# Optimization experiments

Measured on AMD Instinct MI355X. Metric: run time of the kernel, lower is better.

The kernel has to match this reference:

```python
import jax, jax.numpy as jnp
import numpy as np

D_MODEL, N_HEADS, E_LAYERS, D_FF, FACTOR, REP = 128, 8, 5, 64, 3, 128


def setup_inputs() -> dict:
    key = jax.random.key(0)
    ks = jax.random.split(key, 8)
    B, L = 8, 4096
    s = 0.02
    E = E_LAYERS
    def p(k, shape):
        return jax.random.normal(k, shape, jnp.float32) * s
    return dict(
        x=jax.random.normal(ks[0], (B, D_MODEL, L), jnp.float32),
        Wq=p(ks[1], (E, D_MODEL, D_MODEL)), bq=jnp.zeros((E, D_MODEL), jnp.float32),
        Wk=p(ks[2], (E, D_MODEL, D_MODEL)), bk=jnp.zeros((E, D_MODEL), jnp.float32),
        Wv=p(ks[3], (E, D_MODEL, D_MODEL)), bv=jnp.zeros((E, D_MODEL), jnp.float32),
        Wo=p(ks[4], (E, D_MODEL, D_MODEL)), bo=jnp.zeros((E, D_MODEL), jnp.float32),
        W1=p(ks[5], (E, D_FF, D_MODEL)), b1=jnp.zeros((E, D_FF), jnp.float32),
        W2=p(ks[6], (E, D_MODEL, D_FF)), b2=jnp.zeros((E, D_MODEL), jnp.float32),
        ln1_w=jnp.ones((E, D_MODEL), jnp.float32), ln1_b=jnp.zeros((E, D_MODEL), jnp.float32),
        ln2_w=jnp.ones((E, D_MODEL), jnp.float32), ln2_b=jnp.zeros((E, D_MODEL), jnp.float32),
        lnf_w=jnp.ones((D_MODEL,), jnp.float32), lnf_b=jnp.zeros((D_MODEL,), jnp.float32),
        Wp=p(ks[7], (D_MODEL, REP)), bp=jnp.zeros((REP,), jnp.float32),
    )


def _ln(x, w, b, eps=1e-5):
    m = jnp.mean(x, axis=-1, keepdims=True)
    v = jnp.mean((x - m) ** 2, axis=-1, keepdims=True)
    return (x - m) * jax.lax.rsqrt(v + eps) * w + b


def _prob_attn(Q, K, V, key):
    """ProbSparse self-attention (mask_flag=False). Q,K,V: [B,H,L,Eh]."""
    B, H, L, Eh = Q.shape
    c = min(int(FACTOR * np.ceil(np.log(L))), L)  # U_part == u for self-attn
    # sample c keys per query position (shared across batch/head, like torch.randint)
    idx = jax.random.randint(key, (L, c), 0, L)
    Ks = K[:, :, idx, :]                                   # [B,H,L,c,Eh]
    QKs = jnp.einsum('bhle,bhlue->bhlu', Q, Ks)            # sampled scores
    M = QKs.max(-1) - QKs.sum(-1) / L                      # sparsity measure [B,H,L]
    _, top = jax.lax.top_k(M, c)                           # top-u query indices [B,H,c]
    Qr = jnp.take_along_axis(Q, top[..., None], axis=2)    # [B,H,c,Eh]
    scores = jnp.einsum('bhue,bhke->bhuk', Qr, K) * (1.0 / np.sqrt(Eh))
    attn = jax.nn.softmax(scores, axis=-1)                 # [B,H,c,L]
    upd = jnp.einsum('bhuk,bhke->bhue', attn, V)           # [B,H,c,Eh]
    # lazy context: mean of V for non-selected queries
    ctx = jnp.broadcast_to(V.mean(axis=2, keepdims=True), Q.shape)
    bi = jnp.arange(B)[:, None, None]
    hi = jnp.arange(H)[None, :, None]
    ctx = ctx.at[bi, hi, top].set(upd)
    return ctx


def reference(x, Wq, bq, Wk, bk, Wv, bv, Wo, bo, W1, b1, W2, b2,
              ln1_w, ln1_b, ln2_w, ln2_b, lnf_w, lnf_b, Wp, bp):
    B, _, L = x.shape
    Eh = D_MODEL // N_HEADS
    h = jnp.transpose(x, (0, 2, 1))                        # [B,L,D]
    base = jax.random.key(42)
    for l in range(E_LAYERS):
        q = (h @ Wq[l].T + bq[l]).reshape(B, L, N_HEADS, Eh).transpose(0, 2, 1, 3)
        k = (h @ Wk[l].T + bk[l]).reshape(B, L, N_HEADS, Eh).transpose(0, 2, 1, 3)
        v = (h @ Wv[l].T + bv[l]).reshape(B, L, N_HEADS, Eh).transpose(0, 2, 1, 3)
        ctx = _prob_attn(q, k, v, jax.random.fold_in(base, l))
        ctx = ctx.transpose(0, 2, 1, 3).reshape(B, L, D_MODEL)
        h = h + (ctx @ Wo[l].T + bo[l])                    # residual (dropout off)
        h = _ln(h, ln1_w[l], ln1_b[l])
        # 1x1 conv FFN == per-token linear
        y = jax.nn.gelu(h @ W1[l].T + b1[l], approximate=False)
        y = y @ W2[l].T + b2[l]
        h = _ln(h + y, ln2_w[l], ln2_b[l])
    h = _ln(h, lnf_w, lnf_b)
    out = h @ Wp + bp                                      # [B,L,REP]
    return jnp.transpose(out, (0, 2, 1))                   # [B,REP,L]
```

## Files before the change

kernel.cpp:

```cpp
#include <hip/hip_runtime.h>
#include <stdint.h>
#include <math.h>

#define DM   128
#define NH   8
#define EHD  16
#define NLAY 5
#define DFF  64
#define NREP 128
#define NB   8
#define SL   4096
#define NC   27
#define NBH  (NB*NH)
#define NROWS (NB*SL)

typedef _Float16 f16;
typedef f16 f16x8 __attribute__((ext_vector_type(8)));
typedef float f32x16 __attribute__((ext_vector_type(16)));

__device__ __forceinline__ uint32_t rotl32(uint32_t v, int d) {
  return (v << d) | (v >> (32 - d));
}

__device__ __forceinline__ void tf2x32(uint32_t k0, uint32_t k1,
                                       uint32_t x0, uint32_t x1,
                                       uint32_t &o0, uint32_t &o1) {
  uint32_t ks2 = k0 ^ k1 ^ 0x1BD11BDAu;
  x0 += k0; x1 += k1;
#define TFR(r) { x0 += x1; x1 = rotl32(x1, (r)); x1 ^= x0; }
  TFR(13) TFR(15) TFR(26) TFR(6)
  x0 += k1; x1 += ks2 + 1u;
  TFR(17) TFR(29) TFR(16) TFR(24)
  x0 += ks2; x1 += k0 + 2u;
  TFR(13) TFR(15) TFR(26) TFR(6)
  x0 += k0; x1 += k1 + 3u;
  TFR(17) TFR(29) TFR(16) TFR(24)
  x0 += k1; x1 += ks2 + 4u;
  TFR(13) TFR(15) TFR(26) TFR(6)
  x0 += ks2; x1 += k0 + 5u;
#undef TFR
  o0 = x0; o1 = x1;
}

__global__ void gen_bits_kernel(uint32_t* __restrict__ bits, int layer) {
  int i = blockIdx.x * blockDim.x + threadIdx.x;
  if (i >= SL * NC) return;
  uint32_t ka, kb, k2a, k2b, y0, y1;
  tf2x32(0u, 42u, 0u, (uint32_t)layer, ka, kb);
  tf2x32(ka, kb, 0u, 1u, k2a, k2b);
  tf2x32(k2a, k2b, 0u, (uint32_t)i, y0, y1);
  bits[i] = y0 ^ y1;
}

__global__ __launch_bounds__(256) void transpose_x_kernel(const float* __restrict__ x,
                                                          float* __restrict__ h) {
  __shared__ float t[32][33];
  int tid = threadIdx.x;
  int tx = tid & 31, ty = tid >> 5;
  int l0 = blockIdx.x * 32, d0 = blockIdx.y * 32, b = blockIdx.z;
#pragma unroll
  for (int j = 0; j < 4; ++j) {
    int d = d0 + ty + 8 * j;
    t[ty + 8 * j][tx] = x[((size_t)b * DM + d) * SL + l0 + tx];
  }
  __syncthreads();
#pragma unroll
  for (int j = 0; j < 4; ++j) {
    int l = l0 + ty + 8 * j;
    h[((size_t)b * SL + l) * DM + d0 + tx] = t[tx][ty + 8 * j];
  }
}

#define PACK_TOTAL 425984
__global__ __launch_bounds__(256) void prep_weights(
    const float* __restrict__ Wq, const float* __restrict__ Wk,
    const float* __restrict__ Wv, const float* __restrict__ Wo,
    const float* __restrict__ W1, const float* __restrict__ W2,
    const float* __restrict__ Wp, f16* __restrict__ phi, f16* __restrict__ plo) {
  int idx = blockIdx.x * 256 + threadIdx.x;
  if (idx >= PACK_TOTAL) return;
  const float* src; int K, KS16, lsh; int f; bool transp = false;
  if (idx >= 409600) { f = idx - 409600; src = Wp; K = 128; KS16 = 8; lsh = 3; transp = true; }
  else {
    int layer = idx / 81920; int r = idx - layer * 81920;
    if      (r < 16384) { src = Wq + layer * 16384; f = r;         K = 128; KS16 = 8; lsh = 3; }
    else if (r < 32768) { src = Wk + layer * 16384; f = r - 16384; K = 128; KS16 = 8; lsh = 3; }
    else if (r < 49152) { src = Wv + layer * 16384; f = r - 32768; K = 128; KS16 = 8; lsh = 3; }
    else if (r < 65536) { src = Wo + layer * 16384; f = r - 49152; K = 128; KS16 = 8; lsh = 3; }
    else if (r < 73728) { src = W1 + layer * 8192;  f = r - 65536; K = 128; KS16 = 8; lsh = 3; }
    else                { src = W2 + layer * 8192;  f = r - 73728; K = 64;  KS16 = 4; lsh = 2; }
  }
  int j = f & 7, lane = (f >> 3) & 63, rest = f >> 9;
  int ks = rest & (KS16 - 1), nt = rest >> lsh;
  int n = nt * 32 + (lane & 31);
  int kk = ks * 16 + ((lane >> 5) & 1) * 8 + j;
  float x = transp ? src[(size_t)kk * 128 + n] : src[(size_t)n * K + kk];
  f16 h = (f16)x;
  phi[idx] = h;
  plo[idx] = (f16)(x - (float)h);
}

template<int NT32, int KS16, int SRC, int EPI>
__global__ __launch_bounds__(256, 2) void gemm_fused(
    const float* __restrict__ Asrc, const f16* __restrict__ phi,
    const f16* __restrict__ plo,
    const float* __restrict__ bias0, const float* __restrict__ bias1,
    const float* __restrict__ bias2,
    float* out0, float* out1, float* out2,
    const float* __restrict__ gw, const float* __restrict__ gb,
    const float* hres) {
  constexpr int NGW = NT32 / 2;
  constexpr int K = KS16 * 16;
  __shared__ f16x8 Alds[2 * 2 * KS16 * 64];
  __shared__ f16x8 Blds[NT32 * KS16 * 64];
  __shared__ float red[64 * 4];
  int tid = threadIdx.x, lane = tid & 63, wid = tid >> 6;
  int mg = wid >> 1, ng = wid & 1;
  int row0 = blockIdx.x * 64;

  if constexpr (SRC == 0 || SRC == 1) {
    constexpr int OCT = 64 * (K / 8);
    for (int o = tid; o < OCT; o += 256) {
      int row = o / (K / 8);
      int k0 = (o % (K / 8)) * 8;
      float4 f0, f1;
      if constexpr (SRC == 0) {
        const float* s = Asrc + (size_t)(row0 + row) * K + k0;
        f0 = *(const float4*)(s);
        f1 = *(const float4*)(s + 4);
      } else {
        int gr = row0 + row; int bb = gr >> 12, ll = gr & (SL - 1);
        int head = k0 >> 4, e0 = k0 & 15;
        const float* s = Asrc + (((size_t)(bb * NH + head) * SL + ll) * EHD + e0);
        f0 = *(const float4*)(s);
        f1 = *(const float4*)(s + 4);
      }
      f16x8 vh, vl;
      float xs[8] = {f0.x, f0.y, f0.z, f0.w, f1.x, f1.y, f1.z, f1.w};
#pragma unroll
      for (int j = 0; j < 8; ++j) {
        f16 hh = (f16)xs[j];
        vh[j] = hh;
        vl[j] = (f16)(xs[j] - (float)hh);
      }
      int al = (row & 31) | (((k0 >> 3) & 1) << 5);
      int ks = k0 >> 4, mt = row >> 5;
      Alds[((0 * 2 + mt) * KS16 + ks) * 64 + al] = vh;
      Alds[((1 * 2 + mt) * KS16 + ks) * 64 + al] = vl;
    }
  } else {
    int row = tid >> 2, q4 = tid & 3;
    const float* s = Asrc + (size_t)(row0 + row) * 128 + q4 * 32;
    float r[32];
#pragma unroll
    for (int i = 0; i < 8; ++i) {
      float4 f = *(const float4*)(s + 4 * i);
      r[4 * i] = f.x; r[4 * i + 1] = f.y; r[4 * i + 2] = f.z; r[4 * i + 3] = f.w;
    }
    float sm = 0.f, s2 = 0.f;
#pragma unroll
    for (int i = 0; i < 32; ++i) { sm += r[i]; s2 += r[i] * r[i]; }
    sm += __shfl_xor(sm, 1, 4); sm += __shfl_xor(sm, 2, 4);
    s2 += __shfl_xor(s2, 1, 4); s2 += __shfl_xor(s2, 2, 4);
    float mean = sm * (1.f / 128.f);
    float var = s2 * (1.f / 128.f) - mean * mean;
    float rstd = 1.0f / sqrtf(var + 1e-5f);
#pragma unroll
    for (int i = 0; i < 32; ++i) {
      int kk = q4 * 32 + i;
      r[i] = (r[i] - mean) * rstd * gw[kk] + gb[kk];
    }
#pragma unroll
    for (int i = 0; i < 4; ++i) {
      int k0 = q4 * 32 + i * 8;
      f16x8 vh, vl;
#pragma unroll
      for (int j = 0; j < 8; ++j) {
        float x = r[8 * i + j];
        f16 hh = (f16)x;
        vh[j] = hh;
        vl[j] = (f16)(x - (float)hh);
      }
      int al = (row & 31) | (((k0 >> 3) & 1) << 5);
      int ks = k0 >> 4, mt = row >> 5;
      Alds[((0 * 2 + mt) * KS16 + ks) * 64 + al] = vh;
      Alds[((1 * 2 + mt) * KS16 + ks) * 64 + al] = vl;
    }
  }

  constexpr int NMAT = (EPI == 0) ? 3 : 1;
  constexpr int BCNT = NT32 * KS16 * 64;

#define STAGE_B(SRCPTR)                                        \
  {                                                            \
    const float4* bsrc = (const float4*)(SRCPTR);              \
    float4* bdst = (float4*)Blds;                              \
    _Pragma("unroll")                                          \
    for (int i = 0; i < BCNT / 256; ++i) bdst[tid + i * 256] = bsrc[tid + i * 256]; \
  }

#define GEMM_PASS(ASEL)                                                         \
  _Pragma("unroll")                                                             \
  for (int ks = 0; ks < KS16; ++ks) {                                           \
    f16x8 afr = Alds[(((ASEL) * 2 + mg) * KS16 + ks) * 64 + lane];              \
    _Pragma("unroll")                                                           \
    for (int g = 0; g < NGW; ++g) {                                             \
      f16x8 bfr = Blds[((ng * NGW + g) * KS16 + ks) * 64 + lane];               \
      acc[g] = __builtin_amdgcn_mfma_f32_32x32x16_f16(afr, bfr, acc[g], 0, 0, 0); \
    }                                                                           \
  }

  for (int m = 0; m < NMAT; ++m) {
    if (m) __syncthreads();
    STAGE_B(phi + m * 16384)
    __syncthreads();
    f32x16 acc[NGW];
#pragma unroll
    for (int g = 0; g < NGW; ++g)
#pragma unroll
      for (int j = 0; j < 16; ++j) acc[g][j] = 0.f;
    GEMM_PASS(0)
    GEMM_PASS(1)
    __syncthreads();
    STAGE_B(plo + m * 16384)
    __syncthreads();
    GEMM_PASS(0)

    int hi4 = 4 * (lane >> 5);
    if constexpr (EPI == 0) {
      const float* bm = (m == 0) ? bias0 : (m == 1) ? bias1 : bias2;
      float* om = (m == 0) ? out0 : (m == 1) ? out1 : out2;
#pragma unroll
      for (int g = 0; g < NGW; ++g) {
        int col = ng * (NGW * 32) + g * 32 + (lane & 31);
        float bv = bm[col];
        int head = col >> 4, e = col & 15;
#pragma unroll
        for (int reg = 0; reg < 16; ++reg) {
          int row_l = (reg & 3) + 8 * (reg >> 2) + hi4;
          int grow = row0 + mg * 32 + row_l;
          int bb = grow >> 12, ll = grow & (SL - 1);
          om[((size_t)(bb * NH + head) * SL + ll) * EHD + e] = acc[g][reg] + bv;
        }
      }
    } else if constexpr (EPI == 3) {
#pragma unroll
      for (int g = 0; g < NGW; ++g) {
        int col = ng * (NGW * 32) + g * 32 + (lane & 31);
        float bv = bias0[col];
#pragma unroll
        for (int reg = 0; reg < 16; ++reg) {
          int row_l = (reg & 3) + 8 * (reg >> 2) + hi4;
          int grow = row0 + mg * 32 + row_l;
          int bb = grow >> 12, ll = grow & (SL - 1);
          out0[((size_t)(bb * NREP + col)) * SL + ll] = acc[g][reg] + bv;
        }
      }
    } else {
      float bv[2], gwv[2], gbv[2];
#pragma unroll
      for (int g = 0; g < NGW; ++g) {
        int col = ng * (NGW * 32) + g * 32 + (lane & 31);
        bv[g] = bias0[col]; gwv[g] = gw[col]; gbv[g] = gb[col];
      }
      float ps[16], pq[16];
#pragma unroll
      for (int reg = 0; reg < 16; ++reg) {
        int row_l = (reg & 3) + 8 * (reg >> 2) + hi4;
        int grow = row0 + mg * 32 + row_l;
        float vsum = 0.f, qsum = 0.f;
#pragma unroll
        for (int g = 0; g < NGW; ++g) {
          int col = ng * (NGW * 32) + g * 32 + (lane & 31);
          float t = acc[g][reg] + bv[g] + hres[(size_t)grow * DM + col];
          acc[g][reg] = t;
          vsum += t; qsum += t * t;
        }
        vsum += __shfl_xor(vsum, 1, 32); qsum += __shfl_xor(qsum, 1, 32);
        vsum += __shfl_xor(vsum, 2, 32); qsum += __shfl_xor(qsum, 2, 32);
        vsum += __shfl_xor(vsum, 4, 32); qsum += __shfl_xor(qsum, 4, 32);
        vsum += __shfl_xor(vsum, 8, 32); qsum += __shfl_xor(qsum, 8, 32);
        vsum += __shfl_xor(vsum, 16, 32); qsum += __shfl_xor(qsum, 16, 32);
        ps[reg] = vsum; pq[reg] = qsum;
      }
      __syncthreads();
      if ((lane & 31) == 0) {
#pragma unroll
        for (int reg = 0; reg < 16; ++reg) {
          int row_l = (reg & 3) + 8 * (reg >> 2) + hi4;
          int rl = mg * 32 + row_l;
          red[rl * 4 + ng * 2 + 0] = ps[reg];
          red[rl * 4 + ng * 2 + 1] = pq[reg];
        }
      }
      __syncthreads();
#pragma unroll
      for (int reg = 0; reg < 16; ++reg) {
        int row_l = (reg & 3) + 8 * (reg >> 2) + hi4;
        int rl = mg * 32 + row_l;
        int grow = row0 + rl;
        float st = red[rl * 4 + 0] + red[rl * 4 + 2];
        float qt = red[rl * 4 + 1] + red[rl * 4 + 3];
        float mean = st * (1.f / 128.f);
        float var = qt * (1.f / 128.f) - mean * mean;
        float rstd = 1.0f / sqrtf(var + 1e-5f);
#pragma unroll
        for (int g = 0; g < NGW; ++g) {
          int col = ng * (NGW * 32) + g * 32 + (lane & 31);
          out0[(size_t)grow * DM + col] = (acc[g][reg] - mean) * rstd * gwv[g] + gbv[g];
        }
      }
    }
  }
#undef STAGE_B
#undef GEMM_PASS
}

__global__ __launch_bounds__(256, 2) void gemm_ffn(
    const float* __restrict__ h,
    const f16* __restrict__ w1hi, const f16* __restrict__ w1lo,
    const f16* __restrict__ w2hi, const f16* __restrict__ w2lo,
    const float* __restrict__ b1, const float* __restrict__ b2,
    const float* __restrict__ gw, const float* __restrict__ gb,
    float* __restrict__ hout) {
  __shared__ f16x8 AldsH[2 * 2 * 8 * 64];
  __shared__ f16x8 Blds1[2 * 8 * 64];
  __shared__ float ybuf[64 * 64];
  __shared__ float red[64 * 4];
  f16x8* Alds2 = AldsH;
  f16x8* Blds2 = AldsH + 1024;
  int tid = threadIdx.x, lane = tid & 63, wid = tid >> 6;
  int mg = wid >> 1, ng = wid & 1;
  int row0 = blockIdx.x * 64;
  int hi4 = 4 * (lane >> 5);

  for (int o = tid; o < 64 * 16; o += 256) {
    int row = o >> 4;
    int k0 = (o & 15) * 8;
    const float* s = h + (size_t)(row0 + row) * 128 + k0;
    float4 f0 = *(const float4*)(s);
    float4 f1 = *(const float4*)(s + 4);
    f16x8 vh, vl;
    float xs[8] = {f0.x, f0.y, f0.z, f0.w, f1.x, f1.y, f1.z, f1.w};
#pragma unroll
    for (int j = 0; j < 8; ++j) {
      f16 hh = (f16)xs[j];
      vh[j] = hh;
      vl[j] = (f16)(xs[j] - (float)hh);
    }
    int al = (row & 31) | (((k0 >> 3) & 1) << 5);
    int ks = k0 >> 4, mt = row >> 5;
    AldsH[((0 * 2 + mt) * 8 + ks) * 64 + al] = vh;
    AldsH[((1 * 2 + mt) * 8 + ks) * 64 + al] = vl;
  }
  {
    const float4* bsrc = (const float4*)w1hi;
    float4* bdst = (float4*)Blds1;
#pragma unroll
    for (int i = 0; i < 4; ++i) bdst[tid + i * 256] = bsrc[tid + i * 256];
  }
  __syncthreads();
  f32x16 acc1;
#pragma unroll
  for (int j = 0; j < 16; ++j) acc1[j] = 0.f;
#pragma unroll
  for (int asel = 0; asel < 2; ++asel)
#pragma unroll
    for (int ks = 0; ks < 8; ++ks) {
      f16x8 afr = AldsH[((asel * 2 + mg) * 8 + ks) * 64 + lane];
      f16x8 bfr = Blds1[(ng * 8 + ks) * 64 + lane];
      acc1 = __builtin_amdgcn_mfma_f32_32x32x16_f16(afr, bfr, acc1, 0, 0, 0);
    }
  __syncthreads();
  {
    const float4* bsrc = (const float4*)w1lo;
    float4* bdst = (float4*)Blds1;
#pragma unroll
    for (int i = 0; i < 4; ++i) bdst[tid + i * 256] = bsrc[tid + i * 256];
  }
  __syncthreads();
#pragma unroll
  for (int ks = 0; ks < 8; ++ks) {
    f16x8 afr = AldsH[((0 * 2 + mg) * 8 + ks) * 64 + lane];
    f16x8 bfr = Blds1[(ng * 8 + ks) * 64 + lane];
    acc1 = __builtin_amdgcn_mfma_f32_32x32x16_f16(afr, bfr, acc1, 0, 0, 0);
  }
  {
    int col = ng * 32 + (lane & 31);
    float bv = b1[col];
    const float is2 = 0.707106781186547524f;
#pragma unroll
    for (int reg = 0; reg < 16; ++reg) {
      int row_l = (reg & 3) + 8 * (reg >> 2) + hi4 + mg * 32;
      float a = acc1[reg] + bv;
      ybuf[row_l * 64 + col] = 0.5f * a * (1.f + erff(a * is2));
    }
  }
  __syncthreads();
  for (int o = tid; o < 64 * 8; o += 256) {
    int row = o >> 3;
    int k0 = (o & 7) * 8;
    f16x8 vh, vl;
#pragma unroll
    for (int j = 0; j < 8; ++j) {
      float x = ybuf[row * 64 + k0 + j];
      f16 hh = (f16)x;
      vh[j] = hh;
      vl[j] = (f16)(x - (float)hh);
    }
    int al = (row & 31) | (((k0 >> 3) & 1) << 5);
    int ks = k0 >> 4, mt = row >> 5;
    Alds2[((0 * 2 + mt) * 4 + ks) * 64 + al] = vh;
    Alds2[((1 * 2 + mt) * 4 + ks) * 64 + al] = vl;
  }
  {
    const float4* bsrc = (const float4*)w2hi;
    float4* bdst = (float4*)Blds2;
#pragma unroll
    for (int i = 0; i < 4; ++i) bdst[tid + i * 256] = bsrc[tid + i * 256];
  }
  __syncthreads();
  f32x16 acc[2];
#pragma unroll
  for (int g = 0; g < 2; ++g)
#pragma unroll
    for (int j = 0; j < 16; ++j) acc[g][j] = 0.f;
#pragma unroll
  for (int asel = 0; asel < 2; ++asel)
#pragma unroll
    for (int ks = 0; ks < 4; ++ks) {
      f16x8 afr = Alds2[((asel * 2 + mg) * 4 + ks) * 64 + lane];
#pragma unroll
      for (int g = 0; g < 2; ++g) {
        f16x8 bfr = Blds2[((ng * 2 + g) * 4 + ks) * 64 + lane];
        acc[g] = __builtin_amdgcn_mfma_f32_32x32x16_f16(afr, bfr, acc[g], 0, 0, 0);
      }
    }
  __syncthreads();
  {
    const float4* bsrc = (const float4*)w2lo;
    float4* bdst = (float4*)Blds2;
#pragma unroll
    for (int i = 0; i < 4; ++i) bdst[tid + i * 256] = bsrc[tid + i * 256];
  }
  __syncthreads();
#pragma unroll
  for (int ks = 0; ks < 4; ++ks) {
    f16x8 afr = Alds2[((0 * 2 + mg) * 4 + ks) * 64 + lane];
#pragma unroll
    for (int g = 0; g < 2; ++g) {
      f16x8 bfr = Blds2[((ng * 2 + g) * 4 + ks) * 64 + lane];
      acc[g] = __builtin_amdgcn_mfma_f32_32x32x16_f16(afr, bfr, acc[g], 0, 0, 0);
    }
  }
  {
    float bv[2], gwv[2], gbv[2];
#pragma unroll
    for (int g = 0; g < 2; ++g) {
      int col = ng * 64 + g * 32 + (lane & 31);
      bv[g] = b2[col]; gwv[g] = gw[col]; gbv[g] = gb[col];
    }
    float ps[16], pq[16];
#pragma unroll
    for (int reg = 0; reg < 16; ++reg) {
      int row_l = (reg & 3) + 8 * (reg >> 2) + hi4;
      int grow = row0 + mg * 32 + row_l;
      float vsum = 0.f, qsum = 0.f;
#pragma unroll
      for (int g = 0; g < 2; ++g) {
        int col = ng * 64 + g * 32 + (lane & 31);
        float t = acc[g][reg] + bv[g] + h[(size_t)grow * DM + col];
        acc[g][reg] = t;
        vsum += t; qsum += t * t;
      }
      vsum += __shfl_xor(vsum, 1, 32); qsum += __shfl_xor(qsum, 1, 32);
      vsum += __shfl_xor(vsum, 2, 32); qsum += __shfl_xor(qsum, 2, 32);
      vsum += __shfl_xor(vsum, 4, 32); qsum += __shfl_xor(qsum, 4, 32);
      vsum += __shfl_xor(vsum, 8, 32); qsum += __shfl_xor(qsum, 8, 32);
      vsum += __shfl_xor(vsum, 16, 32); qsum += __shfl_xor(qsum, 16, 32);
      ps[reg] = vsum; pq[reg] = qsum;
    }
    __syncthreads();
    if ((lane & 31) == 0) {
#pragma unroll
      for (int reg = 0; reg < 16; ++reg) {
        int row_l = (reg & 3) + 8 * (reg >> 2) + hi4;
        int rl = mg * 32 + row_l;
        red[rl * 4 + ng * 2 + 0] = ps[reg];
        red[rl * 4 + ng * 2 + 1] = pq[reg];
      }
    }
    __syncthreads();
#pragma unroll
    for (int reg = 0; reg < 16; ++reg) {
      int row_l = (reg & 3) + 8 * (reg >> 2) + hi4;
      int rl = mg * 32 + row_l;
      int grow = row0 + rl;
      float st = red[rl * 4 + 0] + red[rl * 4 + 2];
      float qt = red[rl * 4 + 1] + red[rl * 4 + 3];
      float mean = st * (1.f / 128.f);
      float var = qt * (1.f / 128.f) - mean * mean;
      float rstd = 1.0f / sqrtf(var + 1e-5f);
#pragma unroll
      for (int g = 0; g < 2; ++g) {
        int col = ng * 64 + g * 32 + (lane & 31);
        hout[(size_t)grow * DM + col] = (acc[g][reg] - mean) * rstd * gwv[g] + gbv[g];
      }
    }
  }
}

__global__ __launch_bounds__(256) void sampM_kernel(const float* __restrict__ q,
    const float* __restrict__ k, const uint32_t* __restrict__ bits,
    float* __restrict__ M) {
  int tid = threadIdx.x;
  int wave = tid >> 6, lane = tid & 63;
  int bh = blockIdx.x & 63;
  int l = (blockIdx.x >> 6) * 4 + wave;
  int bidx = (lane < NC) ? lane : 0;
  uint32_t bv = bits[l * NC + bidx];
  int u = lane >> 1;
  bool act = (u < NC);
  uint32_t bu = __shfl(bv, u, 64);
  int ki = (int)(bu & (SL - 1));
  int h8 = (lane & 1) * 8;
  const float* kr = k + ((size_t)bh * SL + ki) * EHD + h8;
  float4 k0 = *(const float4*)(kr);
  float4 k1 = *(const float4*)(kr + 4);
  const float* qr = q + ((size_t)bh * SL + l) * EHD + h8;
  float4 q0 = *(const float4*)(qr);
  float4 q1 = *(const float4*)(qr + 4);
  float s = q0.x*k0.x + q0.y*k0.y + q0.z*k0.z + q0.w*k0.w
          + q1.x*k1.x + q1.y*k1.y + q1.z*k1.z + q1.w*k1.w;
  s += __shfl_xor(s, 1, 64);
  float mval = act ? s : -INFINITY;
  float sval = (act && (lane & 1) == 0) ? s : 0.f;
#pragma unroll
  for (int off = 1; off < 64; off <<= 1) {
    mval = fmaxf(mval, __shfl_xor(mval, off, 64));
    sval += __shfl_xor(sval, off, 64);
  }
  if (lane == 0) M[(size_t)bh * SL + l] = mval - sval * (1.0f / (float)SL);
}

__global__ __launch_bounds__(256) void topk_kernel(const float* __restrict__ M,
                                                   int* __restrict__ top) {
  int bh  = blockIdx.x;
  int tid = threadIdx.x;
  int lane = tid & 63, wave = tid >> 6;
  __shared__ float vals[SL];
  __shared__ float wmax[4];
  __shared__ int   widx[4];
  for (int i = tid; i < SL; i += 256) vals[i] = M[(size_t)bh * SL + i];
  __syncthreads();
  for (int u = 0; u < NC; ++u) {
    float bm = -INFINITY; int bi = SL;
#pragma unroll
    for (int j = 0; j < SL / 256; ++j) {
      int i = tid + j * 256;
      float vv = vals[i];
      if (vv > bm) { bm = vv; bi = i; }
    }
#pragma unroll
    for (int off = 32; off > 0; off >>= 1) {
      float v2 = __shfl_xor(bm, off, 64);
      int   i2 = __shfl_xor(bi, off, 64);
      if (v2 > bm || (v2 == bm && i2 < bi)) { bm = v2; bi = i2; }
    }
    if (lane == 0) { wmax[wave] = bm; widx[wave] = bi; }
    __syncthreads();
    if (tid == 0) {
      float b0 = wmax[0]; int x0 = widx[0];
#pragma unroll
      for (int w = 1; w < 4; ++w) {
        float vw = wmax[w]; int iw = widx[w];
        if (vw > b0 || (vw == b0 && iw < x0)) { b0 = vw; x0 = iw; }
      }
      top[bh * NC + u] = x0;
      vals[x0] = -INFINITY;
    }
    __syncthreads();
  }
}

__global__ __launch_bounds__(256) void vmean_part(const float* __restrict__ v,
                                                  float* __restrict__ partial) {
  int bh = blockIdx.x & 63;
  int chunk = blockIdx.x >> 6;
  int tid = threadIdx.x;
  int e = tid & 15, g = tid >> 4;
  const float* vb = v + ((size_t)bh * SL + chunk * 256) * EHD;
  float s = 0.f;
#pragma unroll
  for (int j = 0; j < 16; ++j) s += vb[(size_t)(j * 16 + g) * EHD + e];
  __shared__ float red[256];
  red[tid] = s; __syncthreads();
  for (int st = 128; st >= 16; st >>= 1) {
    if (tid < st) red[tid] += red[tid + st];
    __syncthreads();
  }
  if (tid < EHD) partial[(bh * 16 + chunk) * EHD + tid] = red[tid];
}

__global__ __launch_bounds__(256) void fillctx_kernel(const float* __restrict__ partial,
                                                      float* __restrict__ ctx) {
  __shared__ float vm[EHD];
  int tid = threadIdx.x;
  int t0 = blockIdx.x * 256;
  int bh = t0 >> 14;
  if (tid < EHD) {
    float s = 0.f;
#pragma unroll
    for (int c = 0; c < 16; ++c) s += partial[(bh * 16 + c) * EHD + tid];
    vm[tid] = s * (1.0f / (float)SL);
  }
  __syncthreads();
  int t = t0 + tid;
  int e0 = (t & 3) * 4;
  *(float4*)(ctx + (size_t)t * 4) = make_float4(vm[e0], vm[e0 + 1], vm[e0 + 2], vm[e0 + 3]);
}

__global__ __launch_bounds__(256) void attn_flash(const float* __restrict__ q,
    const float* __restrict__ k, const float* __restrict__ v,
    const int* __restrict__ top, float* __restrict__ ctx) {
  int bh = blockIdx.x & 63, ug = blockIdx.x >> 6;
  int tid = threadIdx.x, wid = tid >> 6, lane = tid & 63;
  int base = ug * 7;
  int nq = (ug < 3) ? 7 : 6;
  bool has0 = (wid < nq);
  bool has1 = (wid + 4 < nq);
  int u0 = base + (has0 ? wid : 0);
  int u1 = base + (has1 ? wid + 4 : 0);
  int qi0 = top[bh * NC + u0];
  int qi1 = top[bh * NC + u1];
  float q0[16], q1[16];
  {
    const float* p0 = q + ((size_t)bh * SL + qi0) * EHD;
    const float* p1 = q + ((size_t)bh * SL + qi1) * EHD;
#pragma unroll
    for (int i = 0; i < 4; ++i) {
      float4 f = *(const float4*)(p0 + 4 * i);
      q0[4*i] = f.x; q0[4*i+1] = f.y; q0[4*i+2] = f.z; q0[4*i+3] = f.w;
      float4 g = *(const float4*)(p1 + 4 * i);
      q1[4*i] = g.x; q1[4*i+1] = g.y; q1[4*i+2] = g.z; q1[4*i+3] = g.w;
    }
  }
  float m0 = -INFINITY, m1 = -INFINITY, l0 = 0.f, l1 = 0.f;
  float a0[16], a1[16];
#pragma unroll
  for (int j = 0; j < 16; ++j) { a0[j] = 0.f; a1[j] = 0.f; }
  const float* kb = k + (size_t)bh * SL * EHD;
  const float* vb = v + (size_t)bh * SL * EHD;
  for (int t = 0; t < 64; ++t) {
    int ki = lane + (t << 6);
    float kr[16], vr[16];
    {
      const float* kp = kb + (size_t)ki * EHD;
      const float* vp = vb + (size_t)ki * EHD;
#pragma unroll
      for (int i = 0; i < 4; ++i) {
        float4 f = *(const float4*)(kp + 4 * i);
        kr[4*i] = f.x; kr[4*i+1] = f.y; kr[4*i+2] = f.z; kr[4*i+3] = f.w;
        float4 g = *(const float4*)(vp + 4 * i);
        vr[4*i] = g.x; vr[4*i+1] = g.y; vr[4*i+2] = g.z; vr[4*i+3] = g.w;
      }
    }
    float s0 = 0.f, s1 = 0.f;
#pragma unroll
    for (int j = 0; j < 16; ++j) { s0 += q0[j] * kr[j]; s1 += q1[j] * kr[j]; }
    s0 *= 0.25f; s1 *= 0.25f;
    {
      float d = s0 - m0;
      float e = expf(-fabsf(d));
      bool gt = d > 0.f;
      float c = gt ? e : 1.f;
      float p = gt ? 1.f : e;
      m0 = gt ? s0 : m0;
      l0 = l0 * c + p;
#pragma unroll
      for (int j = 0; j < 16; ++j) a0[j] = a0[j] * c + p * vr[j];
    }
    {
      float d = s1 - m1;
      float e = expf(-fabsf(d));
      bool gt = d > 0.f;
      float c = gt ? e : 1.f;
      float p = gt ? 1.f : e;
      m1 = gt ? s1 : m1;
      l1 = l1 * c + p;
#pragma unroll
      for (int j = 0; j < 16; ++j) a1[j] = a1[j] * c + p * vr[j];
    }
  }
#pragma unroll
  for (int off = 1; off < 64; off <<= 1) {
    {
      float mo = __shfl_xor(m0, off, 64);
      float lo_ = __shfl_xor(l0, off, 64);
      float mn = fmaxf(m0, mo);
      float cs = expf(m0 - mn), co = expf(mo - mn);
      l0 = l0 * cs + lo_ * co;
#pragma unroll
      for (int j = 0; j < 16; ++j) {
        float ao = __shfl_xor(a0[j], off, 64);
        a0[j] = a0[j] * cs + ao * co;
      }
      m0 = mn;
    }
    {
      float mo = __shfl_xor(m1, off, 64);
      float lo_ = __shfl_xor(l1, off, 64);
      float mn = fmaxf(m1, mo);
      float cs = expf(m1 - mn), co = expf(mo - mn);
      l1 = l1 * cs + lo_ * co;
#pragma unroll
      for (int j = 0; j < 16; ++j) {
        float ao = __shfl_xor(a1[j], off, 64);
        a1[j] = a1[j] * cs + ao * co;
      }
      m1 = mn;
    }
  }
  if (lane == 0 && has0) {
    float inv = 1.0f / l0;
    float* o = ctx + ((size_t)bh * SL + qi0) * EHD;
#pragma unroll
    for (int j = 0; j < 16; ++j) o[j] = a0[j] * inv;
  }
  if (lane == 0 && has1) {
    float inv = 1.0f / l1;
    float* o = ctx + ((size_t)bh * SL + qi1) * EHD;
#pragma unroll
    for (int j = 0; j < 16; ++j) o[j] = a1[j] * inv;
  }
}

extern "C" void kernel_launch(void* const* d_in, const int* in_sizes, int n_in,
                              void* d_out, int out_size, void* d_ws, size_t ws_size,
                              hipStream_t stream) {
  const float* x   = (const float*)d_in[0];
  const float* Wq  = (const float*)d_in[1];
  const float* bq  = (const float*)d_in[2];
  const float* Wk  = (const float*)d_in[3];
  const float* bk  = (const float*)d_in[4];
  const float* Wv  = (const float*)d_in[5];
  const float* bv  = (const float*)d_in[6];
  const float* Wo  = (const float*)d_in[7];
  const float* bo  = (const float*)d_in[8];
  const float* W1  = (const float*)d_in[9];
  const float* b1  = (const float*)d_in[10];
  const float* W2  = (const float*)d_in[11];
  const float* b2  = (const float*)d_in[12];
  const float* ln1w = (const float*)d_in[13];
  const float* ln1b = (const float*)d_in[14];
  const float* ln2w = (const float*)d_in[15];
  const float* ln2b = (const float*)d_in[16];
  const float* lnfw = (const float*)d_in[17];
  const float* lnfb = (const float*)d_in[18];
  const float* Wp  = (const float*)d_in[19];
  const float* bp  = (const float*)d_in[20];
  float* out = (float*)d_out;

  float* ws = (float*)d_ws;
  float* h     = ws;
  float* q     = ws + 4194304;
  float* k     = ws + 8388608;
  float* v     = ws + 12582912;
  float* ctx   = ws + 16777216;
  float* partial = ws + 20971520;
  float* M     = ws + 23068672;
  int*   top   = (int*)(ws + 23331840);
  uint32_t* bits = (uint32_t*)(ws + 23333888);
  f16* phi = (f16*)(ws + 23444480);
  f16* plo = (f16*)(ws + 23657472);

  transpose_x_kernel<<<dim3(SL / 32, DM / 32, NB), 256, 0, stream>>>(x, h);
  prep_weights<<<(PACK_TOTAL + 255) / 256, 256, 0, stream>>>(
      Wq, Wk, Wv, Wo, W1, W2, Wp, phi, plo);

  for (int l = 0; l < NLAY; ++l) {
    size_t lb = (size_t)l * 81920;
    gen_bits_kernel<<<(SL * NC + 255) / 256, 256, 0, stream>>>(bits, l);
    gemm_fused<4, 8, 0, 0><<<NROWS / 64, 256, 0, stream>>>(
        h, phi + lb, plo + lb, bq + l * DM, bk + l * DM, bv + l * DM,
        q, k, v, nullptr, nullptr, nullptr);
    sampM_kernel<<<NBH * SL / 4, 256, 0, stream>>>(q, k, bits, M);
    topk_kernel<<<NBH, 256, 0, stream>>>(M, top);
    vmean_part<<<NBH * 16, 256, 0, stream>>>(v, partial);
    fillctx_kernel<<<NBH * SL * 4 / 256, 256, 0, stream>>>(partial, ctx);
    attn_flash<<<256, 256, 0, stream>>>(q, k, v, top, ctx);
    gemm_fused<4, 8, 1, 1><<<NROWS / 64, 256, 0, stream>>>(
        ctx, phi + lb + 49152, plo + lb + 49152, bo + l * DM, nullptr, nullptr,
        h, nullptr, nullptr, ln1w + l * DM, ln1b + l * DM, h);
    gemm_ffn<<<NROWS / 64, 256, 0, stream>>>(
        h, phi + lb + 65536, plo + lb + 65536,
        phi + lb + 73728, plo + lb + 73728,
        b1 + l * DFF, b2 + l * DM, ln2w + l * DM, ln2b + l * DM, h);
  }

  gemm_fused<4, 8, 3, 3><<<NROWS / 64, 256, 0, stream>>>(
      h, phi + 409600, plo + 409600, bp, nullptr, nullptr,
      out, nullptr, nullptr, lnfw, lnfb, nullptr);
}
```

Measured before the change: 965.3 us.

## Split attention over key chunks and merge partial softmax states

The flash attention kernel now divides the 4096 keys into 4 chunks, launching four times as many blocks. Each block writes its running max, sum and unnormalized accumulator to a scratch buffer, and a new merge kernel combines them with log-sum-exp rescaling. This is meant to fill more of the GPU, since the old 256-block launch under-occupied it, at the cost of an extra launch and some scratch traffic. The sampM kernel also loads the sampled key index directly instead of broadcasting it through a shuffle, and skips the redundant first reduction step.

Measured after the change: 971.9 us. Within noise of the previous version (+0.7%).

```diff
diff --git a/kernel.cpp b/kernel.cpp
--- a/kernel.cpp
+++ b/kernel.cpp
@@ -13,6 +13,7 @@
 #define NC   27
 #define NBH  (NB*NH)
 #define NROWS (NB*SL)
+#define ACH  4
 
 typedef _Float16 f16;
 typedef f16 f16x8 __attribute__((ext_vector_type(8)));
@@ -517,12 +518,10 @@
   int wave = tid >> 6, lane = tid & 63;
   int bh = blockIdx.x & 63;
   int l = (blockIdx.x >> 6) * 4 + wave;
-  int bidx = (lane < NC) ? lane : 0;
-  uint32_t bv = bits[l * NC + bidx];
   int u = lane >> 1;
   bool act = (u < NC);
-  uint32_t bu = __shfl(bv, u, 64);
-  int ki = (int)(bu & (SL - 1));
+  int uc = act ? u : 0;
+  int ki = (int)(bits[l * NC + uc] & (SL - 1));
   int h8 = (lane & 1) * 8;
   const float* kr = k + ((size_t)bh * SL + ki) * EHD + h8;
   float4 k0 = *(const float4*)(kr);
@@ -536,7 +535,7 @@
   float mval = act ? s : -INFINITY;
   float sval = (act && (lane & 1) == 0) ? s : 0.f;
 #pragma unroll
-  for (int off = 1; off < 64; off <<= 1) {
+  for (int off = 2; off < 64; off <<= 1) {
     mval = fmaxf(mval, __shfl_xor(mval, off, 64));
     sval += __shfl_xor(sval, off, 64);
   }
@@ -622,8 +621,8 @@
 
 __global__ __launch_bounds__(256) void attn_flash(const float* __restrict__ q,
     const float* __restrict__ k, const float* __restrict__ v,
-    const int* __restrict__ top, float* __restrict__ ctx) {
-  int bh = blockIdx.x & 63, ug = blockIdx.x >> 6;
+    const int* __restrict__ top, float* __restrict__ pa) {
+  int bh = blockIdx.x & 63, ug = (blockIdx.x >> 6) & 3, chunk = blockIdx.x >> 8;
   int tid = threadIdx.x, wid = tid >> 6, lane = tid & 63;
   int base = ug * 7;
   int nq = (ug < 3) ? 7 : 6;
@@ -651,8 +650,9 @@
   for (int j = 0; j < 16; ++j) { a0[j] = 0.f; a1[j] = 0.f; }
   const float* kb = k + (size_t)bh * SL * EHD;
   const float* vb = v + (size_t)bh * SL * EHD;
-  for (int t = 0; t < 64; ++t) {
-    int ki = lane + (t << 6);
+  int row_base = chunk * (SL / ACH);
+  for (int t = 0; t < SL / ACH / 64; ++t) {
+    int ki = row_base + lane + (t << 6);
     float kr[16], vr[16];
     {
       const float* kp = kb + (size_t)ki * EHD;
@@ -722,17 +722,44 @@
     }
   }
   if (lane == 0 && has0) {
-    float inv = 1.0f / l0;
-    float* o = ctx + ((size_t)bh * SL + qi0) * EHD;
-#pragma unroll
-    for (int j = 0; j < 16; ++j) o[j] = a0[j] * inv;
+    float* o = pa + ((size_t)(bh * NC + u0) * ACH + chunk) * 18;
+    o[0] = m0; o[1] = l0;
+#pragma unroll
+    for (int j = 0; j < 16; ++j) o[2 + j] = a0[j];
   }
   if (lane == 0 && has1) {
-    float inv = 1.0f / l1;
-    float* o = ctx + ((size_t)bh * SL + qi1) * EHD;
-#pragma unroll
-    for (int j = 0; j < 16; ++j) o[j] = a1[j] * inv;
-  }
+    float* o = pa + ((size_t)(bh * NC + u1) * ACH + chunk) * 18;
+    o[0] = m1; o[1] = l1;
+#pragma unroll
+    for (int j = 0; j < 16; ++j) o[2 + j] = a1[j];
+  }
+}
+
+__global__ __launch_bounds__(64) void attn_merge(const float* __restrict__ pa,
+    const int* __restrict__ top, float* __restrict__ ctx) {
+  int bh = blockIdx.x;
+  int u = threadIdx.x;
+  if (u >= NC) return;
+  float m = -INFINITY, L = 0.f;
+  float a[16];
+#pragma unroll
+  for (int j = 0; j < 16; ++j) a[j] = 0.f;
+#pragma unroll
+  for (int c = 0; c < ACH; ++c) {
+    const float* p = pa + ((size_t)(bh * NC + u) * ACH + c) * 18;
+    float pm = p[0], pl = p[1];
+    float mn = fmaxf(m, pm);
+    float cs = expf(m - mn), co = expf(pm - mn);
+    L = L * cs + pl * co;
+#pragma unroll
+    for (int j = 0; j < 16; ++j) a[j] = a[j] * cs + p[2 + j] * co;
+    m = mn;
+  }
+  int qi = top[bh * NC + u];
+  float inv = 1.0f / L;
+  float* o = ctx + ((size_t)bh * SL + qi) * EHD;
+#pragma unroll
+  for (int j = 0; j < 16; ++j) o[j] = a[j] * inv;
 }
 
 extern "C" void kernel_launch(void* const* d_in, const int* in_sizes, int n_in,
@@ -768,6 +795,7 @@
   float* v     = ws + 12582912;
   float* ctx   = ws + 16777216;
   float* partial = ws + 20971520;
+  float* pa    = ws + 20987904;
   float* M     = ws + 23068672;
   int*   top   = (int*)(ws + 23331840);
   uint32_t* bits = (uint32_t*)(ws + 23333888);
@@ -788,7 +816,8 @@
     topk_kernel<<<NBH, 256, 0, stream>>>(M, top);
     vmean_part<<<NBH * 16, 256, 0, stream>>>(v, partial);
     fillctx_kernel<<<NBH * SL * 4 / 256, 256, 0, stream>>>(partial, ctx);
-    attn_flash<<<256, 256, 0, stream>>>(q, k, v, top, ctx);
+    attn_flash<<<ACH * 256, 256, 0, stream>>>(q, k, v, top, pa);
+    attn_merge<<<NBH, 64, 0, stream>>>(pa, top, ctx);
     gemm_fused<4, 8, 1, 1><<<NROWS / 64, 256, 0, stream>>>(
         ctx, phi + lb + 49152, plo + lb + 49152, bo + l * DM, nullptr, nullptr,
         h, nullptr, nullptr, ln1w + l * DM, ln1b + l * DM, h);
```
